# Performance work log

Measured on AMD Instinct MI355X. Metric: run time of the kernel, lower is better.

## Reference

```python
import jax, jax.numpy as jnp
import numpy as np

EPS = 1e-08


def setup_inputs() -> dict:
    key = jax.random.key(0)
    B, E, C = 8192, 8, 1000
    p = jax.random.uniform(key, (B, E, C), dtype=jnp.float32)
    p = p / jnp.sum(p, axis=-1, keepdims=True)  # valid posteriors
    return {"posteriors": p}


def _extract(posteriors):
    B, E, C = posteriors.shape
    p = posteriors
    logp = jnp.log(p + EPS)                              # [B,E,C]
    plogp_sum = jnp.sum(p * logp, axis=-1)               # [B,E]

    expert_entropy = -plogp_sum                          # [B,E]
    expert_confidence = jnp.max(p, axis=-1)              # [B,E]

    top2, _ = jax.lax.top_k(p, 2)                        # C >= 2 here
    expert_margin = top2[..., 0] - top2[..., 1]          # [B,E]

    # disagreement: number of unique argmax classes across experts
    top1 = jnp.argmax(p, axis=-1)                        # [B,E] int
    top1_sorted = jnp.sort(top1, axis=-1)
    n_unique = 1 + jnp.sum(top1_sorted[:, 1:] != top1_sorted[:, :-1], axis=-1)
    disagreement_ratio = (n_unique - 1).astype(p.dtype) / max(E - 1, 1)  # [B]

    # mean pairwise KL over i<j pairs: KL_ij = sum_c p_i*(logp_i - logp_j)
    cross = jnp.einsum('bic,bjc->bij', p, logp)          # [B,E,E]
    kl = plogp_sum[:, :, None] - cross                   # [B,E,E]
    triu = jnp.triu(jnp.ones((E, E), dtype=p.dtype), k=1)
    n_pairs = E * (E - 1) // 2
    mean_pairwise_kl = jnp.sum(kl * triu, axis=(1, 2)) / n_pairs  # [B]

    mixture = jnp.mean(p, axis=1)                        # [B,C]
    mixture_entropy = -jnp.sum(mixture * jnp.log(mixture + EPS), axis=-1)  # [B]

    post_var = jnp.var(p, axis=1, ddof=1).mean(axis=-1)  # [B] (unbiased, as torch.var)
    mutual_info = mixture_entropy - jnp.mean(expert_entropy, axis=-1)      # [B]

    sg = jax.lax.stop_gradient  # torch computes these under @torch.no_grad()
    feats = jnp.concatenate([
        p.reshape(B, E * C),
        sg(expert_entropy),
        sg(expert_confidence),
        sg(expert_margin),
        sg(disagreement_ratio)[:, None],
        sg(mean_pairwise_kl)[:, None],
        sg(mixture_entropy)[:, None],
        sg(post_var)[:, None],
        sg(mutual_info)[:, None],
    ], axis=-1)                                          # [B, E*C + 3E + 5]
    return feats


def reference(posteriors):
    return _extract(posteriors)
```

## Files before the change

kernel.cpp:

```cpp
#include <hip/hip_runtime.h>

#define EPSF 1e-8f

__global__ __launch_bounds__(256, 4) void gating_feat_kernel(
    const float* __restrict__ pin, float* __restrict__ out)
{
    const int b = blockIdx.x;
    const int t = threadIdx.x;
    const size_t inb = (size_t)b * 8000;
    const size_t ob  = (size_t)b * 8029;

    float plogp[8], mx1[8], mx2[8];
    int   am[8];
#pragma unroll
    for (int e = 0; e < 8; ++e) {
        plogp[e] = 0.f; mx1[e] = -3.0e38f; mx2[e] = -3.0e38f; am[e] = 0x7fffffff;
    }
    float cross = 0.f;
    float mixent = 0.f;
    float varacc = 0.f;

    if (t < 250) {
        float pr[8][4];
#pragma unroll
        for (int e = 0; e < 8; ++e)
#pragma unroll
            for (int k = 0; k < 4; ++k)
                pr[e][k] = pin[inb + e * 1000 + k * 250 + t];
#pragma unroll
        for (int e = 0; e < 8; ++e)
#pragma unroll
            for (int k = 0; k < 4; ++k)
                out[ob + e * 1000 + k * 250 + t] = pr[e][k];

#pragma unroll
        for (int k = 0; k < 4; ++k) {
            const int c = k * 250 + t;
            float prefix = 0.f, ss = 0.f;
#pragma unroll
            for (int e = 0; e < 8; ++e) {
                const float pv = pr[e][k];
                const float lp = __logf(pv + EPSF);
                plogp[e] += pv * lp;
                if (pv > mx1[e]) { mx2[e] = mx1[e]; mx1[e] = pv; am[e] = c; }
                else if (pv > mx2[e]) { mx2[e] = pv; }
                cross += prefix * lp;
                prefix += pv;
                ss += pv * pv;
            }
            const float m = prefix * 0.125f;
            mixent += m * __logf(m + EPSF);
            varacc += ss - 8.f * m * m;
        }
    }

#pragma unroll
    for (int off = 32; off >= 1; off >>= 1) {
#pragma unroll
        for (int e = 0; e < 8; ++e) {
            plogp[e] += __shfl_down(plogp[e], off);
            const float o1 = __shfl_down(mx1[e], off);
            const float o2 = __shfl_down(mx2[e], off);
            const int   oa = __shfl_down(am[e], off);
            if (o1 > mx1[e])       { mx2[e] = fmaxf(mx1[e], o2); mx1[e] = o1; am[e] = oa; }
            else if (o1 == mx1[e]) { mx2[e] = mx1[e]; if (oa < am[e]) am[e] = oa; }
            else                   { mx2[e] = fmaxf(mx2[e], o1); }
        }
        cross  += __shfl_down(cross,  off);
        mixent += __shfl_down(mixent, off);
        varacc += __shfl_down(varacc, off);
    }

    __shared__ float sf[4][27];
    __shared__ int   si[4][8];
    const int wave = t >> 6;
    const int lane = t & 63;
    if (lane == 0) {
#pragma unroll
        for (int e = 0; e < 8; ++e) {
            sf[wave][e]      = plogp[e];
            sf[wave][8 + e]  = mx1[e];
            sf[wave][16 + e] = mx2[e];
            si[wave][e]      = am[e];
        }
        sf[wave][24] = cross; sf[wave][25] = mixent; sf[wave][26] = varacc;
    }
    __syncthreads();

    if (t == 0) {
        for (int w = 1; w < 4; ++w) {
#pragma unroll
            for (int e = 0; e < 8; ++e) {
                plogp[e] += sf[w][e];
                const float o1 = sf[w][8 + e], o2 = sf[w][16 + e];
                const int   oa = si[w][e];
                if (o1 > mx1[e])       { mx2[e] = fmaxf(mx1[e], o2); mx1[e] = o1; am[e] = oa; }
                else if (o1 == mx1[e]) { mx2[e] = mx1[e]; if (oa < am[e]) am[e] = oa; }
                else                   { mx2[e] = fmaxf(mx2[e], o1); }
            }
            cross += sf[w][24]; mixent += sf[w][25]; varacc += sf[w][26];
        }

        float sum_plogp = 0.f, wsum = 0.f;
#pragma unroll
        for (int e = 0; e < 8; ++e) {
            sum_plogp += plogp[e];
            wsum += (float)(7 - e) * plogp[e];
            out[ob + 8000 + e] = -plogp[e];
            out[ob + 8008 + e] = mx1[e];
            out[ob + 8016 + e] = mx1[e] - mx2[e];
        }
        int nu = 0;
        for (int i = 0; i < 8; ++i) {
            bool u = true;
            for (int j = 0; j < i; ++j) if (am[j] == am[i]) u = false;
            nu += u ? 1 : 0;
        }
        out[ob + 8024] = (float)(nu - 1) * (1.f / 7.f);
        out[ob + 8025] = (wsum - cross) * (1.f / 28.f);
        const float me = -mixent;
        out[ob + 8026] = me;
        out[ob + 8027] = varacc * (1.f / 7000.f);
        out[ob + 8028] = me + sum_plogp * 0.125f;
    }
}

extern "C" void kernel_launch(void* const* d_in, const int* in_sizes, int n_in,
                              void* d_out, int out_size, void* d_ws, size_t ws_size,
                              hipStream_t stream) {
    const float* p = (const float*)d_in[0];
    float* out = (float*)d_out;
    const int B = in_sizes[0] / 8000;
    gating_feat_kernel<<<B, 256, 0, stream>>>(p, out);
}
```

Before: 510.9 us.

## Map one row per wavefront and drop the block-level reduction

Each wavefront now processes a whole batch row by looping over classes in 64-lane strides. This removes the shared-memory staging and __syncthreads cross-wave reduction. The top-1 value and argmax are packed into a 64-bit key so the butterfly xor-shuffle reduction is branch-light. Logs switch to log2 with a final ln2 rescale, the copied posteriors use nontemporal stores, and launch bounds are raised for occupancy. The trade-off is fewer loads in flight per thread, since only 8 are issued per iteration instead of 32 up front.

```diff
diff --git a/kernel.cpp b/kernel.cpp
--- a/kernel.cpp
+++ b/kernel.cpp
@@ -1,127 +1,109 @@
 #include <hip/hip_runtime.h>
 
 #define EPSF 1e-8f
+#define LN2F 0.69314718055994530942f
 
-__global__ __launch_bounds__(256, 4) void gating_feat_kernel(
-    const float* __restrict__ pin, float* __restrict__ out)
+__global__ __launch_bounds__(256, 6) void gating_feat_kernel(
+    const float* __restrict__ pin, float* __restrict__ out, int B)
 {
-    const int b = blockIdx.x;
-    const int t = threadIdx.x;
-    const size_t inb = (size_t)b * 8000;
-    const size_t ob  = (size_t)b * 8029;
+    const int lane = threadIdx.x & 63;
+    const int b = blockIdx.x * 4 + (threadIdx.x >> 6);
+    if (b >= B) return;
+    const float* __restrict__ rin  = pin + (size_t)b * 8000;
+    float*       __restrict__ rout = out + (size_t)b * 8029;
 
     float plogp[8], mx1[8], mx2[8];
     int   am[8];
 #pragma unroll
     for (int e = 0; e < 8; ++e) {
-        plogp[e] = 0.f; mx1[e] = -3.0e38f; mx2[e] = -3.0e38f; am[e] = 0x7fffffff;
+        plogp[e] = 0.f; mx1[e] = 0.f; mx2[e] = 0.f; am[e] = 0x7fffffff;
     }
     float cross = 0.f;
     float mixent = 0.f;
     float varacc = 0.f;
 
-    if (t < 250) {
-        float pr[8][4];
 #pragma unroll
-        for (int e = 0; e < 8; ++e)
+    for (int s = 0; s < 16; ++s) {
+        const int c = lane + (s << 6);
+        if (s < 15 || lane < 40) {
+            float pr[8];
 #pragma unroll
-            for (int k = 0; k < 4; ++k)
-                pr[e][k] = pin[inb + e * 1000 + k * 250 + t];
+            for (int e = 0; e < 8; ++e)
+                pr[e] = rin[e * 1000 + c];
 #pragma unroll
-        for (int e = 0; e < 8; ++e)
-#pragma unroll
-            for (int k = 0; k < 4; ++k)
-                out[ob + e * 1000 + k * 250 + t] = pr[e][k];
+            for (int e = 0; e < 8; ++e)
+                __builtin_nontemporal_store(pr[e], rout + e * 1000 + c);
 
-#pragma unroll
-        for (int k = 0; k < 4; ++k) {
-            const int c = k * 250 + t;
             float prefix = 0.f, ss = 0.f;
 #pragma unroll
             for (int e = 0; e < 8; ++e) {
-                const float pv = pr[e][k];
-                const float lp = __logf(pv + EPSF);
-                plogp[e] += pv * lp;
-                if (pv > mx1[e]) { mx2[e] = mx1[e]; mx1[e] = pv; am[e] = c; }
-                else if (pv > mx2[e]) { mx2[e] = pv; }
-                cross += prefix * lp;
+                const float pv = pr[e];
+                const float lp = __log2f(pv + EPSF);
+                plogp[e] = __fmaf_rn(pv, lp, plogp[e]);
+                const bool gt = pv > mx1[e];
+                mx2[e] = fmaxf(mx2[e], fminf(pv, mx1[e]));
+                if (gt) { mx1[e] = pv; am[e] = c; }
+                cross  = __fmaf_rn(prefix, lp, cross);
                 prefix += pv;
-                ss += pv * pv;
+                ss     = __fmaf_rn(pv, pv, ss);
             }
             const float m = prefix * 0.125f;
-            mixent += m * __logf(m + EPSF);
+            mixent = __fmaf_rn(m, __log2f(m + EPSF), mixent);
             varacc += ss - 8.f * m * m;
         }
     }
+
+    unsigned long long key[8];
+#pragma unroll
+    for (int e = 0; e < 8; ++e)
+        key[e] = ((unsigned long long)__float_as_uint(mx1[e]) << 32)
+               | (unsigned)(0xFFFFFFFFu - (unsigned)am[e]);
 
 #pragma unroll
     for (int off = 32; off >= 1; off >>= 1) {
 #pragma unroll
         for (int e = 0; e < 8; ++e) {
-            plogp[e] += __shfl_down(plogp[e], off);
-            const float o1 = __shfl_down(mx1[e], off);
-            const float o2 = __shfl_down(mx2[e], off);
-            const int   oa = __shfl_down(am[e], off);
-            if (o1 > mx1[e])       { mx2[e] = fmaxf(mx1[e], o2); mx1[e] = o1; am[e] = oa; }
-            else if (o1 == mx1[e]) { mx2[e] = mx1[e]; if (oa < am[e]) am[e] = oa; }
-            else                   { mx2[e] = fmaxf(mx2[e], o1); }
+            const unsigned long long ok = __shfl_xor(key[e], off);
+            const float o2 = __shfl_xor(mx2[e], off);
+            const float a1 = __uint_as_float((unsigned)(key[e] >> 32));
+            const float b1 = __uint_as_float((unsigned)(ok >> 32));
+            mx2[e] = fmaxf(fmaxf(mx2[e], o2), fminf(a1, b1));
+            if (ok > key[e]) key[e] = ok;
+            plogp[e] += __shfl_xor(plogp[e], off);
         }
-        cross  += __shfl_down(cross,  off);
-        mixent += __shfl_down(mixent, off);
-        varacc += __shfl_down(varacc, off);
+        cross  += __shfl_xor(cross,  off);
+        mixent += __shfl_xor(mixent, off);
+        varacc += __shfl_xor(varacc, off);
     }
 
-    __shared__ float sf[4][27];
-    __shared__ int   si[4][8];
-    const int wave = t >> 6;
-    const int lane = t & 63;
     if (lane == 0) {
+        float sum_plogp = 0.f, wsum = 0.f;
+        int amf[8];
 #pragma unroll
         for (int e = 0; e < 8; ++e) {
-            sf[wave][e]      = plogp[e];
-            sf[wave][8 + e]  = mx1[e];
-            sf[wave][16 + e] = mx2[e];
-            si[wave][e]      = am[e];
-        }
-        sf[wave][24] = cross; sf[wave][25] = mixent; sf[wave][26] = varacc;
-    }
-    __syncthreads();
-
-    if (t == 0) {
-        for (int w = 1; w < 4; ++w) {
-#pragma unroll
-            for (int e = 0; e < 8; ++e) {
-                plogp[e] += sf[w][e];
-                const float o1 = sf[w][8 + e], o2 = sf[w][16 + e];
-                const int   oa = si[w][e];
-                if (o1 > mx1[e])       { mx2[e] = fmaxf(mx1[e], o2); mx1[e] = o1; am[e] = oa; }
-                else if (o1 == mx1[e]) { mx2[e] = mx1[e]; if (oa < am[e]) am[e] = oa; }
-                else                   { mx2[e] = fmaxf(mx2[e], o1); }
-            }
-            cross += sf[w][24]; mixent += sf[w][25]; varacc += sf[w][26];
-        }
-
-        float sum_plogp = 0.f, wsum = 0.f;
-#pragma unroll
-        for (int e = 0; e < 8; ++e) {
-            sum_plogp += plogp[e];
-            wsum += (float)(7 - e) * plogp[e];
-            out[ob + 8000 + e] = -plogp[e];
-            out[ob + 8008 + e] = mx1[e];
-            out[ob + 8016 + e] = mx1[e] - mx2[e];
+            const float pe = plogp[e] * LN2F;
+            sum_plogp += pe;
+            wsum += (float)(7 - e) * pe;
+            const float m1 = __uint_as_float((unsigned)(key[e] >> 32));
+            amf[e] = (int)(0xFFFFFFFFu - (unsigned)(key[e] & 0xFFFFFFFFu));
+            rout[8000 + e] = -pe;
+            rout[8008 + e] = m1;
+            rout[8016 + e] = m1 - mx2[e];
         }
         int nu = 0;
+#pragma unroll
         for (int i = 0; i < 8; ++i) {
             bool u = true;
-            for (int j = 0; j < i; ++j) if (am[j] == am[i]) u = false;
+#pragma unroll
+            for (int j = 0; j < i; ++j) u = u && (amf[j] != amf[i]);
             nu += u ? 1 : 0;
         }
-        out[ob + 8024] = (float)(nu - 1) * (1.f / 7.f);
-        out[ob + 8025] = (wsum - cross) * (1.f / 28.f);
-        const float me = -mixent;
-        out[ob + 8026] = me;
-        out[ob + 8027] = varacc * (1.f / 7000.f);
-        out[ob + 8028] = me + sum_plogp * 0.125f;
+        rout[8024] = (float)(nu - 1) * (1.f / 7.f);
+        rout[8025] = (wsum - cross * LN2F) * (1.f / 28.f);
+        const float me = -mixent * LN2F;
+        rout[8026] = me;
+        rout[8027] = varacc * (1.f / 7000.f);
+        rout[8028] = me + sum_plogp * 0.125f;
     }
 }
 
@@ -131,5 +113,5 @@
     const float* p = (const float*)d_in[0];
     float* out = (float*)d_out;
     const int B = in_sizes[0] / 8000;
-    gating_feat_kernel<<<B, 256, 0, stream>>>(p, out);
+    gating_feat_kernel<<<(B + 3) / 4, 256, 0, stream>>>(p, out, B);
 }
```

Result: slower. 815.1 us (+59.5%).
